# Kernel tuning notes

Hardware: AMD Instinct MI355X
Metric: run time of the kernel (lower is better)

## Reference

```python
import jax, jax.numpy as jnp
import numpy as np

N, E, C, D, H = 50000, 1600000, 50000, 128, 512


def setup_inputs() -> dict:
    key = jax.random.key(0)
    ks = jax.random.split(key, 16)
    s = jnp.float32(0.02)  # keep activations stable through 3 layers
    inp = {}
    inp["x"] = jax.random.normal(ks[0], (N, D), jnp.float32)
    inp["edge_index"] = jax.random.randint(ks[1], (2, E), 0, N)
    inp["first_edge"] = jax.random.randint(ks[2], (2,), 0, N)
    inp["candidate_edges"] = jax.random.randint(ks[3], (C, 2), 0, N)
    inp["t"] = jax.random.uniform(ks[4], (1, 1), jnp.float32)
    dims = [(D, H), (H, H), (H, H)]
    i = 5
    for l, (di, do) in enumerate(dims):
        inp[f"gin{l}_w1"] = jax.random.normal(ks[i], (di, do), jnp.float32) * s; i += 1
        inp[f"gin{l}_b1"] = jnp.zeros((do,), jnp.float32)
        inp[f"gin{l}_w2"] = jax.random.normal(ks[i], (do, do), jnp.float32) * s; i += 1
        inp[f"gin{l}_b2"] = jnp.zeros((do,), jnp.float32)
    inp["pred_w1"] = jax.random.normal(ks[i], (5 * H, H), jnp.float32) * s; i += 1
    inp["pred_b1"] = jnp.zeros((H,), jnp.float32)
    inp["pred_w2"] = jax.random.normal(ks[i], (H, 1), jnp.float32) * s; i += 1
    inp["pred_b2"] = jnp.zeros((1,), jnp.float32)
    inp["time_w1"] = jax.random.normal(ks[i], (1, H), jnp.float32) * s; i += 1
    inp["time_b1"] = jnp.zeros((H,), jnp.float32)
    inp["time_w2"] = jax.random.normal(ks[i], (H, H), jnp.float32) * s; i += 1
    inp["time_b2"] = jnp.zeros((H,), jnp.float32)
    return inp


def _edge_rep(x, u, v):
    # 'sum_absdiff': cat([x_u + x_v, |x_u - x_v|]) -> 2*H features
    xu, xv = x[u], x[v]
    return jnp.concatenate([xu + xv, jnp.abs(xu - xv)], axis=-1)


def reference(x, edge_index, first_edge, candidate_edges, t,
              gin0_w1, gin0_b1, gin0_w2, gin0_b2,
              gin1_w1, gin1_b1, gin1_w2, gin1_b2,
              gin2_w1, gin2_b1, gin2_w2, gin2_b2,
              pred_w1, pred_b1, pred_w2, pred_b2,
              time_w1, time_b1, time_w2, time_b2):
    src, dst = edge_index[0], edge_index[1]
    layers = [(gin0_w1, gin0_b1, gin0_w2, gin0_b2),
              (gin1_w1, gin1_b1, gin1_w2, gin1_b2),
              (gin2_w1, gin2_b1, gin2_w2, gin2_b2)]
    # GINConv (eps=0): h_i = MLP(x_i + sum_{j->i} x_j)
    for w1, b1, w2, b2 in layers:
        agg = jax.ops.segment_sum(x[src], dst, num_segments=x.shape[0])
        h = x + agg
        x = jax.nn.relu(h @ w1 + b1) @ w2 + b2
    first_feat = _edge_rep(x, first_edge[0], first_edge[1])  # [2H]
    t_embed = (jax.nn.relu(t @ time_w1 + time_b1) @ time_w2 + time_b2)[0]  # [H]
    cand_feat = _edge_rep(x, candidate_edges[:, 0], candidate_edges[:, 1])  # [C, 2H]
    Cn = cand_feat.shape[0]
    feat = jnp.concatenate([
        jnp.broadcast_to(first_feat, (Cn, first_feat.shape[0])),
        cand_feat,
        jnp.broadcast_to(t_embed, (Cn, t_embed.shape[0])),
    ], axis=-1)  # [C, 5H]
    logits = (jax.nn.relu(feat @ pred_w1 + pred_b1) @ pred_w2 + pred_b2)[:, 0]  # [C]
    return logits
```

## Files before the change

kernel.cpp:

```cpp
#include <hip/hip_runtime.h>

typedef __bf16 bf16x2 __attribute__((ext_vector_type(2)));
typedef __bf16 bf16x4 __attribute__((ext_vector_type(4)));
typedef __bf16 bf16x8 __attribute__((ext_vector_type(8)));
typedef float f32x4 __attribute__((ext_vector_type(4)));

#define LDSTR 40

__global__ void hist_kernel(const int* __restrict__ dst, int* __restrict__ deg, int E) {
    int i = blockIdx.x * 256 + threadIdx.x;
    if (i < E) atomicAdd(&deg[dst[i]], 1);
}

__global__ __launch_bounds__(1024)
void scan_kernel(const int* __restrict__ deg, int* __restrict__ rowptr,
                 int* __restrict__ cursor, int n) {
    __shared__ int part[1024];
    int tid = threadIdx.x;
    int chunk = (n + 1023) >> 10;
    int beg = tid * chunk;
    int fin = min(beg + chunk, n);
    int s = 0;
    for (int i = beg; i < fin; i++) s += deg[i];
    part[tid] = s;
    __syncthreads();
    for (int off = 1; off < 1024; off <<= 1) {
        int v = (tid >= off) ? part[tid - off] : 0;
        __syncthreads();
        part[tid] += v;
        __syncthreads();
    }
    int run = (tid == 0) ? 0 : part[tid - 1];
    for (int i = beg; i < fin; i++) {
        rowptr[i] = run; cursor[i] = run; run += deg[i];
    }
    if (tid == 1023) rowptr[n] = run;
}

__global__ void scatter_kernel(const int* __restrict__ src, const int* __restrict__ dst,
                               int* __restrict__ cursor, int* __restrict__ colsrc, int E) {
    int i = blockIdx.x * 256 + threadIdx.x;
    if (i < E) {
        int p = atomicAdd(&cursor[dst[i]], 1);
        colsrc[p] = src[i];
    }
}

__global__ void f32_to_bf16_kernel(const float* __restrict__ in, __bf16* __restrict__ out, int n4) {
    int i = blockIdx.x * 256 + threadIdx.x;
    if (i < n4) {
        float4 f = ((const float4*)in)[i];
        bf16x4 o;
        o[0] = (__bf16)f.x; o[1] = (__bf16)f.y; o[2] = (__bf16)f.z; o[3] = (__bf16)f.w;
        ((bf16x4*)out)[i] = o;
    }
}

__global__ void wprep_kernel(const float* __restrict__ in, __bf16* __restrict__ out, int kbits) {
    int idx = blockIdx.x * 256 + threadIdx.x;
    int K = 1 << kbits;
    if (idx < (512 << kbits)) {
        int k = idx & (K - 1);
        int n = idx >> kbits;
        out[idx] = (__bf16)in[k * 512 + n];
    }
}

template<int F>
__global__ __launch_bounds__(256)
void agg_kernel(const __bf16* __restrict__ xb, const int* __restrict__ rowptr,
                const int* __restrict__ colsrc, __bf16* __restrict__ h, int n) {
    const int node = blockIdx.x * 4 + (threadIdx.x >> 6);
    if (node >= n) return;
    const int lane = threadIdx.x & 63;
    const int DIM = F * 64;
    float acc[F];
    {
        const __bf16* p = xb + (size_t)node * DIM + lane * F;
        if constexpr (F == 8) {
            bf16x8 v = *(const bf16x8*)p;
            #pragma unroll
            for (int i = 0; i < 8; i++) acc[i] = (float)v[i];
        } else {
            bf16x2 v = *(const bf16x2*)p;
            acc[0] = (float)v[0]; acc[1] = (float)v[1];
        }
    }
    int e = rowptr[node], end = rowptr[node + 1];
    for (; e + 2 <= end; e += 2) {
        int s0 = colsrc[e], s1 = colsrc[e + 1];
        const __bf16* p0 = xb + (size_t)s0 * DIM + lane * F;
        const __bf16* p1 = xb + (size_t)s1 * DIM + lane * F;
        if constexpr (F == 8) {
            bf16x8 v0 = *(const bf16x8*)p0;
            bf16x8 v1 = *(const bf16x8*)p1;
            #pragma unroll
            for (int i = 0; i < 8; i++) acc[i] += (float)v0[i] + (float)v1[i];
        } else {
            bf16x2 v0 = *(const bf16x2*)p0;
            bf16x2 v1 = *(const bf16x2*)p1;
            acc[0] += (float)v0[0] + (float)v1[0];
            acc[1] += (float)v0[1] + (float)v1[1];
        }
    }
    if (e < end) {
        int s0 = colsrc[e];
        const __bf16* p0 = xb + (size_t)s0 * DIM + lane * F;
        if constexpr (F == 8) {
            bf16x8 v0 = *(const bf16x8*)p0;
            #pragma unroll
            for (int i = 0; i < 8; i++) acc[i] += (float)v0[i];
        } else {
            bf16x2 v0 = *(const bf16x2*)p0;
            acc[0] += (float)v0[0]; acc[1] += (float)v0[1];
        }
    }
    __bf16* out = h + (size_t)node * DIM + lane * F;
    if constexpr (F == 8) {
        bf16x8 o;
        #pragma unroll
        for (int i = 0; i < 8; i++) o[i] = (__bf16)acc[i];
        *(bf16x8*)out = o;
    } else {
        bf16x2 o; o[0] = (__bf16)acc[0]; o[1] = (__bf16)acc[1];
        *(bf16x2*)out = o;
    }
}

template<int AMODE, bool RELU>
__global__ __launch_bounds__(256, 3)
void gemm_kernel(const __bf16* __restrict__ A, const __bf16* __restrict__ Xb,
                 const int* __restrict__ cand, const __bf16* __restrict__ Bt,
                 const float* __restrict__ bias, __bf16* __restrict__ Cout,
                 int M, int K) {
    __shared__ __bf16 sA[64 * LDSTR];
    __shared__ __bf16 sB[256 * LDSTR];

    const int tid = threadIdx.x;
    const int lane = tid & 63;
    const int waveN = tid >> 6;
    const int mlane = lane & 15;
    const int quad = lane >> 4;
    const int rowBase = blockIdx.x * 64;
    const int nBase = blockIdx.y * 256;

    const int ar = tid >> 2;
    const int ac = (tid & 3) << 3;
    const int br = tid >> 2;
    const int bc = (tid & 3) << 3;

    const f32x4 fzero = {0.f, 0.f, 0.f, 0.f};
    f32x4 acc[4][4];
    #pragma unroll
    for (int i = 0; i < 4; i++)
        #pragma unroll
        for (int j = 0; j < 4; j++) acc[i][j] = fzero;

    int uu = 0, vv = 0;
    const int grow = rowBase + ar;
    if (AMODE == 1 && grow < M) { uu = cand[2 * grow]; vv = cand[2 * grow + 1]; }

    for (int k0 = 0; k0 < K; k0 += 32) {
        __syncthreads();
        {
            bf16x8 av = {};
            if (AMODE == 0) {
                if (grow < M) av = *(const bf16x8*)(A + (size_t)grow * K + k0 + ac);
            } else {
                if (grow < M) {
                    int k = k0 + ac;
                    int kk = k & 511;
                    bf16x8 xu = *(const bf16x8*)(Xb + (size_t)uu * 512 + kk);
                    bf16x8 xv = *(const bf16x8*)(Xb + (size_t)vv * 512 + kk);
                    if (k < 512) {
                        #pragma unroll
                        for (int q = 0; q < 8; q++) av[q] = (__bf16)((float)xu[q] + (float)xv[q]);
                    } else {
                        #pragma unroll
                        for (int q = 0; q < 8; q++) av[q] = (__bf16)fabsf((float)xu[q] - (float)xv[q]);
                    }
                }
            }
            *(bf16x8*)(sA + ar * LDSTR + ac) = av;
        }
        #pragma unroll
        for (int i = 0; i < 4; i++) {
            int nn = br + i * 64;
            bf16x8 b = *(const bf16x8*)(Bt + (size_t)(nBase + nn) * K + k0 + bc);
            *(bf16x8*)(sB + nn * LDSTR + bc) = b;
        }
        __syncthreads();

        bf16x8 aF[4], bF[4];
        #pragma unroll
        for (int mt = 0; mt < 4; mt++)
            aF[mt] = *(const bf16x8*)(sA + (mt * 16 + mlane) * LDSTR + quad * 8);
        #pragma unroll
        for (int nt = 0; nt < 4; nt++)
            bF[nt] = *(const bf16x8*)(sB + (waveN * 64 + nt * 16 + mlane) * LDSTR + quad * 8);
        #pragma unroll
        for (int mt = 0; mt < 4; mt++)
            #pragma unroll
            for (int nt = 0; nt < 4; nt++)
                acc[mt][nt] = __builtin_amdgcn_mfma_f32_16x16x32_bf16(aF[mt], bF[nt], acc[mt][nt], 0, 0, 0);
    }

    #pragma unroll
    for (int mt = 0; mt < 4; mt++) {
        #pragma unroll
        for (int nt = 0; nt < 4; nt++) {
            int col = nBase + waveN * 64 + nt * 16 + mlane;
            float bv = bias[col];
            #pragma unroll
            for (int r = 0; r < 4; r++) {
                int row = rowBase + mt * 16 + quad * 4 + r;
                if (row < M) {
                    float v = acc[mt][nt][r] + bv;
                    if (RELU) v = fmaxf(v, 0.f);
                    Cout[(size_t)row * 512 + col] = (__bf16)v;
                }
            }
        }
    }
}

__global__ __launch_bounds__(512)
void constvec_kernel(const __bf16* __restrict__ xb, const int* __restrict__ first_edge,
                     const float* __restrict__ t,
                     const float* __restrict__ tw1, const float* __restrict__ tb1,
                     const float* __restrict__ tw2, const float* __restrict__ tb2,
                     const float* __restrict__ pw1, const float* __restrict__ pb1,
                     float* __restrict__ cvec) {
    __shared__ float z1[512];
    __shared__ float te[512];
    __shared__ float ff[1024];
    int tid = threadIdx.x;
    float tv = t[0];
    z1[tid] = fmaxf(tv * tw1[tid] + tb1[tid], 0.f);
    int u = first_edge[0], v = first_edge[1];
    float xu = (float)xb[(size_t)u * 512 + tid];
    float xv = (float)xb[(size_t)v * 512 + tid];
    ff[tid] = xu + xv;
    ff[512 + tid] = fabsf(xu - xv);
    __syncthreads();
    float s = tb2[tid];
    for (int j = 0; j < 512; j++) s += z1[j] * tw2[j * 512 + tid];
    te[tid] = s;
    __syncthreads();
    float c = pb1[tid];
    for (int k = 0; k < 1024; k++) c += ff[k] * pw1[k * 512 + tid];
    for (int j = 0; j < 512; j++) c += te[j] * pw1[(2048 + j) * 512 + tid];
    cvec[tid] = c;
}

__global__ __launch_bounds__(256)
void logits_kernel(const __bf16* __restrict__ Z, const float* __restrict__ w2,
                   const float* __restrict__ b2, float* __restrict__ out, int C) {
    int c = blockIdx.x * 4 + (threadIdx.x >> 6);
    if (c >= C) return;
    int lane = threadIdx.x & 63;
    bf16x8 z = *(const bf16x8*)(Z + (size_t)c * 512 + lane * 8);
    const float4* w = (const float4*)(w2 + lane * 8);
    float4 w0 = w[0], w1 = w[1];
    float s = (float)z[0] * w0.x + (float)z[1] * w0.y + (float)z[2] * w0.z + (float)z[3] * w0.w
            + (float)z[4] * w1.x + (float)z[5] * w1.y + (float)z[6] * w1.z + (float)z[7] * w1.w;
    #pragma unroll
    for (int off = 32; off > 0; off >>= 1) s += __shfl_down(s, off);
    if (lane == 0) out[c] = s + b2[0];
}

extern "C" void kernel_launch(void* const* d_in, const int* in_sizes, int n_in,
                              void* d_out, int out_size, void* d_ws, size_t ws_size,
                              hipStream_t stream) {
    (void)n_in; (void)out_size; (void)ws_size;
    const float* x          = (const float*)d_in[0];
    const int*   edge_index = (const int*)d_in[1];
    const int*   first_edge = (const int*)d_in[2];
    const int*   cand       = (const int*)d_in[3];
    const float* t          = (const float*)d_in[4];
    const float* gw1[3] = {(const float*)d_in[5], (const float*)d_in[9],  (const float*)d_in[13]};
    const float* gb1[3] = {(const float*)d_in[6], (const float*)d_in[10], (const float*)d_in[14]};
    const float* gw2[3] = {(const float*)d_in[7], (const float*)d_in[11], (const float*)d_in[15]};
    const float* gb2[3] = {(const float*)d_in[8], (const float*)d_in[12], (const float*)d_in[16]};
    const float* pw1 = (const float*)d_in[17];
    const float* pb1 = (const float*)d_in[18];
    const float* pw2 = (const float*)d_in[19];
    const float* pb2 = (const float*)d_in[20];
    const float* tw1 = (const float*)d_in[21];
    const float* tb1 = (const float*)d_in[22];
    const float* tw2 = (const float*)d_in[23];
    const float* tb2 = (const float*)d_in[24];

    const int N = in_sizes[0] / 128;
    const int E = in_sizes[1] / 2;
    const int C = in_sizes[3] / 2;

    char* p = (char*)d_ws;
    auto alloc = [&](size_t bytes) -> void* {
        void* r = (void*)p;
        p += (bytes + 255) & ~(size_t)255;
        return r;
    };
    __bf16* h    = (__bf16*)alloc((size_t)N * 512 * 2);
    __bf16* u    = (__bf16*)alloc((size_t)N * 512 * 2);
    __bf16* xb   = (__bf16*)alloc((size_t)N * 512 * 2);
    __bf16* wt01 = (__bf16*)alloc((size_t)512 * 128 * 2);
    __bf16* wt02 = (__bf16*)alloc((size_t)512 * 512 * 2);
    __bf16* wt11 = (__bf16*)alloc((size_t)512 * 512 * 2);
    __bf16* wt12 = (__bf16*)alloc((size_t)512 * 512 * 2);
    __bf16* wt21 = (__bf16*)alloc((size_t)512 * 512 * 2);
    __bf16* wt22 = (__bf16*)alloc((size_t)512 * 512 * 2);
    __bf16* wtH  = (__bf16*)alloc((size_t)512 * 1024 * 2);
    int* rowptr = (int*)alloc((size_t)(N + 1) * 4);
    int* deg    = (int*)alloc((size_t)N * 4);
    int* cursor = (int*)alloc((size_t)N * 4);
    int* colsrc = (int*)alloc((size_t)E * 4);
    float* cvec = (float*)alloc(512 * 4);
    __bf16* xb0 = (__bf16*)u;

    const int* src = edge_index;
    const int* dst = edge_index + E;

    hipMemsetAsync(deg, 0, (size_t)N * 4, stream);
    int eb = (E + 255) / 256;
    hist_kernel<<<eb, 256, 0, stream>>>(dst, deg, E);
    scan_kernel<<<1, 1024, 0, stream>>>(deg, rowptr, cursor, N);
    scatter_kernel<<<eb, 256, 0, stream>>>(src, dst, cursor, colsrc, E);

    f32_to_bf16_kernel<<<((N * 128 / 4) + 255) / 256, 256, 0, stream>>>(x, xb0, N * 128 / 4);
    wprep_kernel<<<((512 << 7)  + 255) / 256, 256, 0, stream>>>(gw1[0], wt01, 7);
    wprep_kernel<<<((512 << 9)  + 255) / 256, 256, 0, stream>>>(gw2[0], wt02, 9);
    wprep_kernel<<<((512 << 9)  + 255) / 256, 256, 0, stream>>>(gw1[1], wt11, 9);
    wprep_kernel<<<((512 << 9)  + 255) / 256, 256, 0, stream>>>(gw2[1], wt12, 9);
    wprep_kernel<<<((512 << 9)  + 255) / 256, 256, 0, stream>>>(gw1[2], wt21, 9);
    wprep_kernel<<<((512 << 9)  + 255) / 256, 256, 0, stream>>>(gw2[2], wt22, 9);
    wprep_kernel<<<((512 << 10) + 255) / 256, 256, 0, stream>>>(pw1 + (size_t)1024 * 512, wtH, 10);

    dim3 ggrid((N + 63) / 64, 2);
    int ablocks = (N + 3) / 4;

    agg_kernel<2><<<ablocks, 256, 0, stream>>>(xb0, rowptr, colsrc, h, N);
    gemm_kernel<0, true ><<<ggrid, 256, 0, stream>>>(h, nullptr, nullptr, wt01, gb1[0], u,  N, 128);
    gemm_kernel<0, false><<<ggrid, 256, 0, stream>>>(u, nullptr, nullptr, wt02, gb2[0], xb, N, 512);
    agg_kernel<8><<<ablocks, 256, 0, stream>>>(xb, rowptr, colsrc, h, N);
    gemm_kernel<0, true ><<<ggrid, 256, 0, stream>>>(h, nullptr, nullptr, wt11, gb1[1], u,  N, 512);
    gemm_kernel<0, false><<<ggrid, 256, 0, stream>>>(u, nullptr, nullptr, wt12, gb2[1], xb, N, 512);
    agg_kernel<8><<<ablocks, 256, 0, stream>>>(xb, rowptr, colsrc, h, N);
    gemm_kernel<0, true ><<<ggrid, 256, 0, stream>>>(h, nullptr, nullptr, wt21, gb1[2], u,  N, 512);
    gemm_kernel<0, false><<<ggrid, 256, 0, stream>>>(u, nullptr, nullptr, wt22, gb2[2], xb, N, 512);

    constvec_kernel<<<1, 512, 0, stream>>>(xb, first_edge, t, tw1, tb1, tw2, tb2, pw1, pb1, cvec);
    dim3 hgrid((C + 63) / 64, 2);
    gemm_kernel<1, true><<<hgrid, 256, 0, stream>>>(nullptr, xb, cand, wtH, cvec, u, C, 1024);
    logits_kernel<<<(C + 3) / 4, 256, 0, stream>>>(u, pw2, pb2, (float*)d_out, C);
}
```

Baseline: 1.479 ms.

## Widen GEMM blocks to full 512-column output and unroll aggregation by four

The GEMM kernel now uses 512-thread blocks that each compute all 512 output columns for a 64-row tile, replacing the previous 2-block split along N. Each A tile is therefore loaded, and in the candidate mode gathered and combined, only once instead of twice, though each block holds twice as much B in shared memory and fewer blocks fit per CU. The aggregation loop is also unrolled to four neighbor loads per iteration to raise memory-level parallelism, with a scalar remainder loop.

```diff
diff --git a/kernel.cpp b/kernel.cpp
--- a/kernel.cpp
+++ b/kernel.cpp
@@ -87,23 +87,26 @@
         }
     }
     int e = rowptr[node], end = rowptr[node + 1];
-    for (; e + 2 <= end; e += 2) {
-        int s0 = colsrc[e], s1 = colsrc[e + 1];
-        const __bf16* p0 = xb + (size_t)s0 * DIM + lane * F;
-        const __bf16* p1 = xb + (size_t)s1 * DIM + lane * F;
+    for (; e + 4 <= end; e += 4) {
+        int s0 = colsrc[e], s1 = colsrc[e + 1], s2 = colsrc[e + 2], s3 = colsrc[e + 3];
         if constexpr (F == 8) {
-            bf16x8 v0 = *(const bf16x8*)p0;
-            bf16x8 v1 = *(const bf16x8*)p1;
-            #pragma unroll
-            for (int i = 0; i < 8; i++) acc[i] += (float)v0[i] + (float)v1[i];
+            bf16x8 v0 = *(const bf16x8*)(xb + (size_t)s0 * DIM + lane * F);
+            bf16x8 v1 = *(const bf16x8*)(xb + (size_t)s1 * DIM + lane * F);
+            bf16x8 v2 = *(const bf16x8*)(xb + (size_t)s2 * DIM + lane * F);
+            bf16x8 v3 = *(const bf16x8*)(xb + (size_t)s3 * DIM + lane * F);
+            #pragma unroll
+            for (int i = 0; i < 8; i++)
+                acc[i] += ((float)v0[i] + (float)v1[i]) + ((float)v2[i] + (float)v3[i]);
         } else {
-            bf16x2 v0 = *(const bf16x2*)p0;
-            bf16x2 v1 = *(const bf16x2*)p1;
-            acc[0] += (float)v0[0] + (float)v1[0];
-            acc[1] += (float)v0[1] + (float)v1[1];
-        }
-    }
-    if (e < end) {
+            bf16x2 v0 = *(const bf16x2*)(xb + (size_t)s0 * DIM + lane * F);
+            bf16x2 v1 = *(const bf16x2*)(xb + (size_t)s1 * DIM + lane * F);
+            bf16x2 v2 = *(const bf16x2*)(xb + (size_t)s2 * DIM + lane * F);
+            bf16x2 v3 = *(const bf16x2*)(xb + (size_t)s3 * DIM + lane * F);
+            acc[0] += ((float)v0[0] + (float)v1[0]) + ((float)v2[0] + (float)v3[0]);
+            acc[1] += ((float)v0[1] + (float)v1[1]) + ((float)v2[1] + (float)v3[1]);
+        }
+    }
+    for (; e < end; e++) {
         int s0 = colsrc[e];
         const __bf16* p0 = xb + (size_t)s0 * DIM + lane * F;
         if constexpr (F == 8) {
@@ -128,13 +131,13 @@
 }
 
 template<int AMODE, bool RELU>
-__global__ __launch_bounds__(256, 3)
+__global__ __launch_bounds__(512, 2)
 void gemm_kernel(const __bf16* __restrict__ A, const __bf16* __restrict__ Xb,
                  const int* __restrict__ cand, const __bf16* __restrict__ Bt,
                  const float* __restrict__ bias, __bf16* __restrict__ Cout,
                  int M, int K) {
     __shared__ __bf16 sA[64 * LDSTR];
-    __shared__ __bf16 sB[256 * LDSTR];
+    __shared__ __bf16 sB[512 * LDSTR];
 
     const int tid = threadIdx.x;
     const int lane = tid & 63;
@@ -142,10 +145,9 @@
     const int mlane = lane & 15;
     const int quad = lane >> 4;
     const int rowBase = blockIdx.x * 64;
-    const int nBase = blockIdx.y * 256;
-
-    const int ar = tid >> 2;
-    const int ac = (tid & 3) << 3;
+
+    const int ar = tid >> 3;
+    const int ac = (tid & 7) << 2;
     const int br = tid >> 2;
     const int bc = (tid & 3) << 3;
 
@@ -163,30 +165,30 @@
     for (int k0 = 0; k0 < K; k0 += 32) {
         __syncthreads();
         {
-            bf16x8 av = {};
+            bf16x4 av = {};
             if (AMODE == 0) {
-                if (grow < M) av = *(const bf16x8*)(A + (size_t)grow * K + k0 + ac);
+                if (grow < M) av = *(const bf16x4*)(A + (size_t)grow * K + k0 + ac);
             } else {
                 if (grow < M) {
                     int k = k0 + ac;
                     int kk = k & 511;
-                    bf16x8 xu = *(const bf16x8*)(Xb + (size_t)uu * 512 + kk);
-                    bf16x8 xv = *(const bf16x8*)(Xb + (size_t)vv * 512 + kk);
+                    bf16x4 xu = *(const bf16x4*)(Xb + (size_t)uu * 512 + kk);
+                    bf16x4 xv = *(const bf16x4*)(Xb + (size_t)vv * 512 + kk);
                     if (k < 512) {
                         #pragma unroll
-                        for (int q = 0; q < 8; q++) av[q] = (__bf16)((float)xu[q] + (float)xv[q]);
+                        for (int q = 0; q < 4; q++) av[q] = (__bf16)((float)xu[q] + (float)xv[q]);
                     } else {
                         #pragma unroll
-                        for (int q = 0; q < 8; q++) av[q] = (__bf16)fabsf((float)xu[q] - (float)xv[q]);
+                        for (int q = 0; q < 4; q++) av[q] = (__bf16)fabsf((float)xu[q] - (float)xv[q]);
                     }
                 }
             }
-            *(bf16x8*)(sA + ar * LDSTR + ac) = av;
+            *(bf16x4*)(sA + ar * LDSTR + ac) = av;
         }
         #pragma unroll
         for (int i = 0; i < 4; i++) {
-            int nn = br + i * 64;
-            bf16x8 b = *(const bf16x8*)(Bt + (size_t)(nBase + nn) * K + k0 + bc);
+            int nn = br + i * 128;
+            bf16x8 b = *(const bf16x8*)(Bt + (size_t)nn * K + k0 + bc);
             *(bf16x8*)(sB + nn * LDSTR + bc) = b;
         }
         __syncthreads();
@@ -209,7 +211,7 @@
     for (int mt = 0; mt < 4; mt++) {
         #pragma unroll
         for (int nt = 0; nt < 4; nt++) {
-            int col = nBase + waveN * 64 + nt * 16 + mlane;
+            int col = waveN * 64 + nt * 16 + mlane;
             float bv = bias[col];
             #pragma unroll
             for (int r = 0; r < 4; r++) {
@@ -336,21 +338,21 @@
     wprep_kernel<<<((512 << 9)  + 255) / 256, 256, 0, stream>>>(gw2[2], wt22, 9);
     wprep_kernel<<<((512 << 10) + 255) / 256, 256, 0, stream>>>(pw1 + (size_t)1024 * 512, wtH, 10);
 
-    dim3 ggrid((N + 63) / 64, 2);
+    int gblocks = (N + 63) / 64;
     int ablocks = (N + 3) / 4;
 
     agg_kernel<2><<<ablocks, 256, 0, stream>>>(xb0, rowptr, colsrc, h, N);
-    gemm_kernel<0, true ><<<ggrid, 256, 0, stream>>>(h, nullptr, nullptr, wt01, gb1[0], u,  N, 128);
-    gemm_kernel<0, false><<<ggrid, 256, 0, stream>>>(u, nullptr, nullptr, wt02, gb2[0], xb, N, 512);
+    gemm_kernel<0, true ><<<gblocks, 512, 0, stream>>>(h, nullptr, nullptr, wt01, gb1[0], u,  N, 128);
+    gemm_kernel<0, false><<<gblocks, 512, 0, stream>>>(u, nullptr, nullptr, wt02, gb2[0], xb, N, 512);
     agg_kernel<8><<<ablocks, 256, 0, stream>>>(xb, rowptr, colsrc, h, N);
-    gemm_kernel<0, true ><<<ggrid, 256, 0, stream>>>(h, nullptr, nullptr, wt11, gb1[1], u,  N, 512);
-    gemm_kernel<0, false><<<ggrid, 256, 0, stream>>>(u, nullptr, nullptr, wt12, gb2[1], xb, N, 512);
+    gemm_kernel<0, true ><<<gblocks, 512, 0, stream>>>(h, nullptr, nullptr, wt11, gb1[1], u,  N, 512);
+    gemm_kernel<0, false><<<gblocks, 512, 0, stream>>>(u, nullptr, nullptr, wt12, gb2[1], xb, N, 512);
     agg_kernel<8><<<ablocks, 256, 0, stream>>>(xb, rowptr, colsrc, h, N);
-    gemm_kernel<0, true ><<<ggrid, 256, 0, stream>>>(h, nullptr, nullptr, wt21, gb1[2], u,  N, 512);
-    gemm_kernel<0, false><<<ggrid, 256, 0, stream>>>(u, nullptr, nullptr, wt22, gb2[2], xb, N, 512);
+    gemm_kernel<0, true ><<<gblocks, 512, 0, stream>>>(h, nullptr, nullptr, wt21, gb1[2], u,  N, 512);
+    gemm_kernel<0, false><<<gblocks, 512, 0, stream>>>(u, nullptr, nullptr, wt22, gb2[2], xb, N, 512);
 
     constvec_kernel<<<1, 512, 0, stream>>>(xb, first_edge, t, tw1, tb1, tw2, tb2, pw1, pb1, cvec);
-    dim3 hgrid((C + 63) / 64, 2);
-    gemm_kernel<1, true><<<hgrid, 256, 0, stream>>>(nullptr, xb, cand, wtH, cvec, u, C, 1024);
+    int hblocks = (C + 63) / 64;
+    gemm_kernel<1, true><<<hblocks, 512, 0, stream>>>(nullptr, xb, cand, wtH, cvec, u, C, 1024);
     logits_kernel<<<(C + 3) / 4, 256, 0, stream>>>(u, pw2, pb2, (float*)d_out, C);
 }
```

Result: no change. 1.482 ms (+0.2%).
